# Performance work log

Hardware: AMD Instinct MI355X
Metric: run time of the kernel (lower is better)

The kernel has to match this reference:

```python
import jax, jax.numpy as jnp
import numpy as np

N, E, F, H, D, G = 50000, 800000, 64, 256, 64, 128
MIN_SCORE, TOL, EPS = 0.05, 1e-7, 1e-14


def setup_inputs() -> dict:
    key = jax.random.key(0)
    ks = jax.random.split(key, 10)
    x = jax.random.normal(ks[0], (N, F), jnp.float32)
    edge_index = jax.random.randint(ks[1], (2, E), 0, N, dtype=jnp.int32)
    # sorted graph ids, every graph non-empty (PyG batching layout)
    batch = (jnp.arange(N, dtype=jnp.int32) * G // N).astype(jnp.int32)
    na = jax.random.uniform(ks[2], (N,), jnp.float32) + 1e-3
    na = na / jax.ops.segment_sum(na, batch, G)[batch]  # per-graph distribution

    def lin(k, i, o):
        return jax.random.normal(k, (i, o), jnp.float32) / jnp.sqrt(i)

    return dict(
        x=x, node_attention=na,
        W1a=lin(ks[3], F, H), b1a=jnp.zeros((H,), jnp.float32),
        W1b=lin(ks[4], H, D), b1b=jnp.zeros((D,), jnp.float32),
        pw=jax.random.normal(ks[5], (F,), jnp.float32) / jnp.sqrt(F),
        W2a=lin(ks[6], D, H), b2a=jnp.zeros((H,), jnp.float32),
        W2b=lin(ks[7], H, D), b2b=jnp.zeros((D,), jnp.float32),
        Wl=lin(ks[8], D, 1), bl=jnp.zeros((1,), jnp.float32),
        edge_index=edge_index, batch=batch,
    )


def _forward(x, node_attention, W1a, b1a, W1b, b1b, pw, W2a, b2a, W2b, b2b,
             Wl, bl, edge_index, batch):
    src, dst = edge_index[0], edge_index[1]

    def gin(h, Wa, ba, Wb, bb):
        # GINConv (eps=0): nn(x + sum_{j->i} x_j), nn = Linear-ReLU-Linear, then outer ReLU
        agg = jax.ops.segment_sum(h[src], dst, N)
        z = h + agg
        return jax.nn.relu(jax.nn.relu(z @ Wa + ba) @ Wb + bb)

    h1 = gin(x, W1a, b1a, W1b, b1b)                       # [N, 64]

    # TopKPooling with min_score: score = softmax(attn @ w, batch)
    s = x @ pw                                            # attn_input = x_input
    smax = jax.ops.segment_max(s, batch, G)
    e = jnp.exp(s - smax[batch])
    score = e / jax.ops.segment_sum(e, batch, G)[batch]   # per-graph softmax
    # keep nodes with score > min(per-graph max - tol, min_score)  (>=1 node/graph)
    thresh = jnp.minimum(jax.ops.segment_max(score, batch, G)[batch] - TOL, MIN_SCORE)
    mask = score > thresh
    mf = mask.astype(x.dtype)
    xp = h1 * (score * mf)[:, None]                       # x[perm] * score[perm], masked layout
    ratio = mf.sum() / N

    # conv2 on pooled graph: edges survive iff both endpoints kept
    emask = (mf[src] * mf[dst])[:, None]
    agg2 = jax.ops.segment_sum(xp[src] * emask, dst, N)
    h2 = jax.nn.relu(jax.nn.relu((xp + agg2) @ W2a + b2a) @ W2b + b2b) * mf[:, None]

    # gsum readout + linear head
    xg = jax.ops.segment_sum(h2, batch, G) @ Wl + bl      # [G, 1]

    # attn loss: kl_div(log(score+eps), node_attention[perm]) scatter_mean over kept nodes
    t = node_attention
    tlogt = jnp.where(t > 0, t * jnp.log(jnp.where(t > 0, t, 1.0)), 0.0)
    kl = tlogt - t * jnp.log(score + EPS)
    cnt = jnp.maximum(jax.ops.segment_sum(mf, batch, G), 1.0)
    attn_loss = jax.ops.segment_sum(kl * mf, batch, G) / cnt  # [G]

    return xg, attn_loss, ratio


def reference(x, node_attention, W1a, b1a, W1b, b1b, pw, W2a, b2a, W2b, b2b,
              Wl, bl, edge_index, batch):
    return _forward(x, node_attention, W1a, b1a, W1b, b1b, pw, W2a, b2a,
                    W2b, b2b, Wl, bl, edge_index, batch)
```

## Files before the change

### kernel.cpp

```cpp
#include <hip/hip_runtime.h>

constexpr int NN = 50000;
constexpr int EE = 800000;
constexpr int FF = 64;
constexpr int HH = 256;
constexpr int DD = 64;
constexpr int GG = 128;
constexpr int MAXK = 32;
constexpr int MAXQ = 128;
constexpr float MIN_SCORE = 0.05f;
constexpr float TOL = 1e-7f;
constexpr float EPSV = 1e-14f;

__global__ __launch_bounds__(1024) void k_pool(
        const float4* __restrict__ x4, const float4* __restrict__ pw4,
        const float* __restrict__ na,
        int* __restrict__ kept_i, float* __restrict__ kscore,
        int* __restrict__ kcnt, int* __restrict__ ecnt,
        float* __restrict__ aggc, float* __restrict__ out) {
    int g = blockIdx.x;
    int start = (g * NN + GG - 1) / GG;
    int end   = ((g + 1) * NN + GG - 1) / GG;
    int cnt = end - start;
    int t = threadIdx.x;
    int wid = t >> 6, lane = t & 63;
    __shared__ float ev[400];
    __shared__ float red[16];
    __shared__ float sh_smax, sh_esum, sh_kl;
    __shared__ int sh_cnt;

    if (g == 0 && t == 0) *ecnt = 0;
    if (t == 0) { sh_kl = 0.f; sh_cnt = 0; }

    int grp = t >> 4, l4 = t & 15;
    float4 pv = pw4[l4];
    for (int r = grp; r < cnt; r += 64) {
        float4 xv = x4[(size_t)(start + r) * 16 + l4];
        float v = xv.x * pv.x + xv.y * pv.y + xv.z * pv.z + xv.w * pv.w;
#pragma unroll
        for (int off = 1; off < 16; off <<= 1) v += __shfl_xor(v, off);
        if (l4 == 0) ev[r] = v;
    }
    __syncthreads();

    float m = (t < cnt) ? ev[t] : -3.4e38f;
#pragma unroll
    for (int off = 32; off; off >>= 1) m = fmaxf(m, __shfl_xor(m, off));
    if (lane == 0) red[wid] = m;
    __syncthreads();
    if (t == 0) {
        float mm = red[0];
#pragma unroll
        for (int j = 1; j < 16; ++j) mm = fmaxf(mm, red[j]);
        sh_smax = mm;
    }
    __syncthreads();
    float smax = sh_smax;

    float e = (t < cnt) ? expf(ev[t] - smax) : 0.f;
    float ssum = e;
#pragma unroll
    for (int off = 32; off; off >>= 1) ssum += __shfl_xor(ssum, off);
    if (lane == 0) red[wid] = ssum;
    __syncthreads();
    if (t == 0) {
        float s16 = red[0];
#pragma unroll
        for (int j = 1; j < 16; ++j) s16 += red[j];
        sh_esum = s16;
    }
    __syncthreads();
    float esum = sh_esum;

    float thresh = fminf(1.0f / esum - TOL, MIN_SCORE);

    if (t < cnt) {
        int i = start + t;
        float sc = e / esum;
        if (sc > thresh) {
            int rank = atomicAdd(&sh_cnt, 1);
            if (rank < MAXK) {
                int cslot = g * MAXK + rank;
                kept_i[cslot] = i;
                kscore[cslot] = sc;
            }
            float tt = na[i];
            float tlogt = (tt > 0.f) ? tt * logf(tt) : 0.f;
            atomicAdd(&sh_kl, tlogt - tt * logf(sc + EPSV));
        }
    }
    __syncthreads();
    int kc = sh_cnt < MAXK ? sh_cnt : MAXK;
    for (int wdx = t; wdx < kc * DD; wdx += 1024)
        aggc[(size_t)g * MAXK * DD + wdx] = 0.f;
    if (t == 0) {
        kcnt[g] = kc;
        out[GG + g] = sh_kl / (float)(sh_cnt > 0 ? sh_cnt : 1);
    }
}

__global__ __launch_bounds__(256) void k_edge(
        const int* __restrict__ ei, const float* __restrict__ x,
        const int* __restrict__ kept_i, const int* __restrict__ kcnt,
        float* __restrict__ aggc, int* __restrict__ elist,
        int* __restrict__ ecnt) {
    __shared__ int sh_kcnt[GG];
    __shared__ int sh_kid[GG * MAXK];
    int t = threadIdx.x;
    for (int j = t; j < GG; j += 256) sh_kcnt[j] = kcnt[j];
    for (int j = t; j < GG * MAXK; j += 256) sh_kid[j] = kept_i[j];
    __syncthreads();

    int e = blockIdx.x * 256 + t;
    int lane = t & 63;
    int dn = ei[EE + e];
    int gd = (dn * GG) / NN;
    int cd = -1;
    int kcd = sh_kcnt[gd];
    for (int j = 0; j < kcd; ++j)
        if (sh_kid[gd * MAXK + j] == dn) { cd = gd * MAXK + j; break; }

    int sn = 0;
    if (cd >= 0) sn = ei[e];

    unsigned long long hits = __ballot(cd >= 0);
    while (hits) {
        int src_lane = __ffsll(hits) - 1;
        hits &= hits - 1;
        int ecd = __shfl(cd, src_lane);
        int esn = __shfl(sn, src_lane);
        float v = x[(size_t)esn * FF + lane];
        atomicAdd(&aggc[(size_t)ecd * DD + lane], v);
    }

    if (cd >= 0) {
        int gs = (sn * GG) / NN;
        int cs = -1;
        int kcs = sh_kcnt[gs];
        for (int j = 0; j < kcs; ++j)
            if (sh_kid[gs * MAXK + j] == sn) { cs = gs * MAXK + j; break; }
        if (cs >= 0) {
            int j = atomicAdd(ecnt, 1);
            elist[2 * j] = cs;
            elist[2 * j + 1] = cd;
        }
    }
}

__global__ __launch_bounds__(256) void k_tail2(
        const float* __restrict__ x, const int* __restrict__ kept_i,
        const float* __restrict__ kscore, const int* __restrict__ kcnt,
        const int* __restrict__ elist, const int* __restrict__ ecnt,
        const float* __restrict__ aggc,
        const float* __restrict__ W1a, const float* __restrict__ b1a,
        const float* __restrict__ W1b, const float* __restrict__ b1b,
        const float* __restrict__ W2a, const float* __restrict__ b2a,
        const float* __restrict__ W2b, const float* __restrict__ b2b,
        const float* __restrict__ Wl, const float* __restrict__ bl,
        float* __restrict__ out) {
    int g = blockIdx.x;
    int t = threadIdx.x;
    __shared__ float z1[FF], z2[DD], hid[HH], part[4][DD];
    __shared__ int q_cs[MAXQ], q_cd[MAXQ];
    __shared__ int qn, redk[GG];
    __shared__ float gsum_sh;

    if (g == 0) {
        if (t < GG) redk[t] = kcnt[t];
        __syncthreads();
        if (t == 0) {
            int s = 0;
#pragma unroll
            for (int j = 0; j < GG; ++j) s += redk[j];
            out[2 * GG] = (float)s / (float)NN;
        }
    }

    int kc = kcnt[g];
    int lo = g * MAXK, hi = lo + kc;
    if (t == 0) { qn = 0; gsum_sh = 0.f; }
    __syncthreads();

    int en = *ecnt;
    for (int j = t; j < en; j += 256) {
        int cd = elist[2 * j + 1];
        if (cd >= lo && cd < hi) {
            int pos = atomicAdd(&qn, 1);
            if (pos < MAXQ) { q_cs[pos] = elist[2 * j]; q_cd[pos] = cd; }
        }
    }
    __syncthreads();
    int nq = qn < MAXQ ? qn : MAXQ;

    int d = t & 63, qw = t >> 6;

    auto mlp1_accum = [&](int cs) {
        __syncthreads();
        if (t < FF) z1[t] = x[(size_t)kept_i[cs] * FF + t] + aggc[(size_t)cs * DD + t];
        __syncthreads();
        float a = b1a[t];
#pragma unroll 16
        for (int f = 0; f < FF; ++f) a += z1[f] * W1a[f * HH + t];
        hid[t] = fmaxf(a, 0.f);
        __syncthreads();
        float acc = 0.f;
#pragma unroll 16
        for (int h = 0; h < HH / 4; ++h)
            acc += hid[qw * 64 + h] * W1b[(qw * 64 + h) * DD + d];
        part[qw][d] = acc;
        __syncthreads();
        if (t < DD)
            z2[t] += fmaxf(b1b[t] + part[0][t] + part[1][t] + part[2][t] + part[3][t],
                           0.f) * kscore[cs];
    };

    for (int r = 0; r < kc; ++r) {
        int c = lo + r;
        if (t < DD) z2[t] = 0.f;
        mlp1_accum(c);
        for (int j = 0; j < nq; ++j)
            if (q_cd[j] == c) mlp1_accum(q_cs[j]);
        __syncthreads();

        float a = b2a[t];
#pragma unroll 16
        for (int f = 0; f < DD; ++f) a += z2[f] * W2a[f * HH + t];
        hid[t] = fmaxf(a, 0.f);
        __syncthreads();
        float acc = 0.f;
#pragma unroll 16
        for (int h = 0; h < HH / 4; ++h)
            acc += hid[qw * 64 + h] * W2b[(qw * 64 + h) * DD + d];
        part[qw][d] = acc;
        __syncthreads();
        if (t < DD) {
            float v = fmaxf(b2b[t] + part[0][t] + part[1][t] + part[2][t] + part[3][t],
                            0.f);
            float p = v * Wl[t];
#pragma unroll
            for (int off = 1; off < 64; off <<= 1) p += __shfl_xor(p, off);
            if (t == 0) gsum_sh += p;
        }
        __syncthreads();
    }
    if (t == 0) out[g] = gsum_sh + bl[0];
}

extern "C" void kernel_launch(void* const* d_in, const int* in_sizes, int n_in,
                              void* d_out, int out_size, void* d_ws, size_t ws_size,
                              hipStream_t stream) {
    const float* x   = (const float*)d_in[0];
    const float* na  = (const float*)d_in[1];
    const float* W1a = (const float*)d_in[2];
    const float* b1a = (const float*)d_in[3];
    const float* W1b = (const float*)d_in[4];
    const float* b1b = (const float*)d_in[5];
    const float* pw  = (const float*)d_in[6];
    const float* W2a = (const float*)d_in[7];
    const float* b2a = (const float*)d_in[8];
    const float* W2b = (const float*)d_in[9];
    const float* b2b = (const float*)d_in[10];
    const float* Wl  = (const float*)d_in[11];
    const float* bl  = (const float*)d_in[12];
    const int* ei    = (const int*)d_in[13];
    float* out = (float*)d_out;

    char* w = (char*)d_ws;
    auto alloc = [&](size_t bytes) -> void* {
        void* p = (void*)w;
        w += (bytes + 255) & ~(size_t)255;
        return p;
    };
    int*   ecnt    = (int*)alloc(4);
    int*   kcnt    = (int*)alloc(GG * 4);
    int*   kept_i  = (int*)alloc((size_t)GG * MAXK * 4);
    float* kscore  = (float*)alloc((size_t)GG * MAXK * 4);
    float* aggc    = (float*)alloc((size_t)GG * MAXK * DD * 4);
    int*   elist   = (int*)alloc((size_t)2 * EE * 4);
    (void)ws_size; (void)in_sizes; (void)n_in; (void)out_size;

    k_pool<<<GG, 1024, 0, stream>>>((const float4*)x, (const float4*)pw, na,
                                    kept_i, kscore, kcnt, ecnt, aggc, out);
    k_edge<<<EE / 256, 256, 0, stream>>>(ei, x, kept_i, kcnt, aggc, elist, ecnt);
    k_tail2<<<GG, 256, 0, stream>>>(x, kept_i, kscore, kcnt, elist, ecnt,
                                    aggc, W1a, b1a, W1b, b1b,
                                    W2a, b2a, W2b, b2b, Wl, bl, out);
}
```

Baseline: 29.12 us.

## Use per-graph kept-node bitmask and process four edges per thread in edge kernel

The pooling kernel now writes a per-graph bitmask of kept nodes, so the edge kernel can reject most destination nodes with one global load instead of a linear search. The edge kernel no longer stages all kept ids into shared memory per block. Each thread handles four edges via an int4 load, which cuts the block count by a factor of four. The cost is extra global lookups of kcnt/kept_i for the few hits, plus fewer blocks to hide latency.

```diff
diff --git a/kernel.cpp b/kernel.cpp
--- a/kernel.cpp
+++ b/kernel.cpp
@@ -8,6 +8,7 @@
 constexpr int GG = 128;
 constexpr int MAXK = 32;
 constexpr int MAXQ = 128;
+constexpr int WPG = 16;
 constexpr float MIN_SCORE = 0.05f;
 constexpr float TOL = 1e-7f;
 constexpr float EPSV = 1e-14f;
@@ -16,8 +17,9 @@
         const float4* __restrict__ x4, const float4* __restrict__ pw4,
         const float* __restrict__ na,
         int* __restrict__ kept_i, float* __restrict__ kscore,
-        int* __restrict__ kcnt, int* __restrict__ ecnt,
-        float* __restrict__ aggc, float* __restrict__ out) {
+        int* __restrict__ kcnt, unsigned* __restrict__ kmask,
+        int* __restrict__ ecnt, float* __restrict__ aggc,
+        float* __restrict__ out) {
     int g = blockIdx.x;
     int start = (g * NN + GG - 1) / GG;
     int end   = ((g + 1) * NN + GG - 1) / GG;
@@ -28,9 +30,11 @@
     __shared__ float red[16];
     __shared__ float sh_smax, sh_esum, sh_kl;
     __shared__ int sh_cnt;
+    __shared__ unsigned shmask[WPG];
 
     if (g == 0 && t == 0) *ecnt = 0;
     if (t == 0) { sh_kl = 0.f; sh_cnt = 0; }
+    if (t < WPG) shmask[t] = 0u;
 
     int grp = t >> 4, l4 = t & 15;
     float4 pv = pw4[l4];
@@ -83,6 +87,7 @@
                 int cslot = g * MAXK + rank;
                 kept_i[cslot] = i;
                 kscore[cslot] = sc;
+                atomicOr(&shmask[t >> 5], 1u << (t & 31));
             }
             float tt = na[i];
             float tlogt = (tt > 0.f) ? tt * logf(tt) : 0.f;
@@ -91,6 +96,7 @@
     }
     __syncthreads();
     int kc = sh_cnt < MAXK ? sh_cnt : MAXK;
+    if (t < WPG) kmask[g * WPG + t] = shmask[t];
     for (int wdx = t; wdx < kc * DD; wdx += 1024)
         aggc[(size_t)g * MAXK * DD + wdx] = 0.f;
     if (t == 0) {
@@ -102,47 +108,52 @@
 __global__ __launch_bounds__(256) void k_edge(
         const int* __restrict__ ei, const float* __restrict__ x,
         const int* __restrict__ kept_i, const int* __restrict__ kcnt,
+        const unsigned* __restrict__ kmask,
         float* __restrict__ aggc, int* __restrict__ elist,
         int* __restrict__ ecnt) {
-    __shared__ int sh_kcnt[GG];
-    __shared__ int sh_kid[GG * MAXK];
     int t = threadIdx.x;
-    for (int j = t; j < GG; j += 256) sh_kcnt[j] = kcnt[j];
-    for (int j = t; j < GG * MAXK; j += 256) sh_kid[j] = kept_i[j];
-    __syncthreads();
-
-    int e = blockIdx.x * 256 + t;
     int lane = t & 63;
-    int dn = ei[EE + e];
-    int gd = (dn * GG) / NN;
-    int cd = -1;
-    int kcd = sh_kcnt[gd];
-    for (int j = 0; j < kcd; ++j)
-        if (sh_kid[gd * MAXK + j] == dn) { cd = gd * MAXK + j; break; }
-
-    int sn = 0;
-    if (cd >= 0) sn = ei[e];
-
-    unsigned long long hits = __ballot(cd >= 0);
-    while (hits) {
-        int src_lane = __ffsll(hits) - 1;
-        hits &= hits - 1;
-        int ecd = __shfl(cd, src_lane);
-        int esn = __shfl(sn, src_lane);
-        float v = x[(size_t)esn * FF + lane];
-        atomicAdd(&aggc[(size_t)ecd * DD + lane], v);
-    }
-
-    if (cd >= 0) {
-        int gs = (sn * GG) / NN;
-        int cs = -1;
-        int kcs = sh_kcnt[gs];
-        for (int j = 0; j < kcs; ++j)
-            if (sh_kid[gs * MAXK + j] == sn) { cs = gs * MAXK + j; break; }
-        if (cs >= 0) {
-            int j = atomicAdd(ecnt, 1);
-            elist[2 * j] = cs;
-            elist[2 * j + 1] = cd;
+    int e4 = blockIdx.x * 256 + t;
+    bool valid = e4 < EE / 4;
+    int4 dv = {0, 0, 0, 0};
+    if (valid) dv = ((const int4*)(ei + EE))[e4];
+    int ds[4] = {dv.x, dv.y, dv.z, dv.w};
+
+    auto keep_slot = [&](int node) -> int {
+        int gph = (node * GG) / NN;
+        int st = (gph * NN + GG - 1) / GG;
+        int local = node - st;
+        unsigned wm = kmask[gph * WPG + (local >> 5)];
+        if (!((wm >> (local & 31)) & 1u)) return -1;
+        int kcd = kcnt[gph];
+        for (int j = 0; j < kcd; ++j)
+            if (kept_i[gph * MAXK + j] == node) return gph * MAXK + j;
+        return -1;
+    };
+
+#pragma unroll
+    for (int k = 0; k < 4; ++k) {
+        int cd = -1;
+        if (valid) cd = keep_slot(ds[k]);
+        int sn = (cd >= 0) ? ei[e4 * 4 + k] : 0;
+
+        unsigned long long hits = __ballot(cd >= 0);
+        while (hits) {
+            int src_lane = __ffsll(hits) - 1;
+            hits &= hits - 1;
+            int ecd = __shfl(cd, src_lane);
+            int esn = __shfl(sn, src_lane);
+            float v = x[(size_t)esn * FF + lane];
+            atomicAdd(&aggc[(size_t)ecd * DD + lane], v);
+        }
+
+        if (cd >= 0) {
+            int cs = keep_slot(sn);
+            if (cs >= 0) {
+                int j = atomicAdd(ecnt, 1);
+                elist[2 * j] = cs;
+                elist[2 * j + 1] = cd;
+            }
         }
     }
 }
@@ -271,17 +282,19 @@
         w += (bytes + 255) & ~(size_t)255;
         return p;
     };
-    int*   ecnt    = (int*)alloc(4);
-    int*   kcnt    = (int*)alloc(GG * 4);
-    int*   kept_i  = (int*)alloc((size_t)GG * MAXK * 4);
-    float* kscore  = (float*)alloc((size_t)GG * MAXK * 4);
-    float* aggc    = (float*)alloc((size_t)GG * MAXK * DD * 4);
-    int*   elist   = (int*)alloc((size_t)2 * EE * 4);
+    int*      ecnt   = (int*)alloc(4);
+    int*      kcnt   = (int*)alloc(GG * 4);
+    int*      kept_i = (int*)alloc((size_t)GG * MAXK * 4);
+    float*    kscore = (float*)alloc((size_t)GG * MAXK * 4);
+    unsigned* kmask  = (unsigned*)alloc((size_t)GG * WPG * 4);
+    float*    aggc   = (float*)alloc((size_t)GG * MAXK * DD * 4);
+    int*      elist  = (int*)alloc((size_t)2 * EE * 4);
     (void)ws_size; (void)in_sizes; (void)n_in; (void)out_size;
 
     k_pool<<<GG, 1024, 0, stream>>>((const float4*)x, (const float4*)pw, na,
-                                    kept_i, kscore, kcnt, ecnt, aggc, out);
-    k_edge<<<EE / 256, 256, 0, stream>>>(ei, x, kept_i, kcnt, aggc, elist, ecnt);
+                                    kept_i, kscore, kcnt, kmask, ecnt, aggc, out);
+    k_edge<<<(EE / 4 + 255) / 256, 256, 0, stream>>>(ei, x, kept_i, kcnt, kmask,
+                                                     aggc, elist, ecnt);
     k_tail2<<<GG, 256, 0, stream>>>(x, kept_i, kscore, kcnt, elist, ecnt,
                                     aggc, W1a, b1a, W1b, b1b,
                                     W2a, b2a, W2b, b2b, Wl, bl, out);
```

Measured after the change: 28.06 us (median of 2 runs). 1.04x faster.
